# Kernel optimization log

Measured on AMD Instinct MI355X. Metric: run time of the kernel, lower is better.

Reference implementation:

```python
import jax, jax.numpy as jnp
import numpy as np

EMBED = 1024
HEADS = 16
HEAD_DIM = EMBED // HEADS


def setup_inputs() -> dict:
    key = jax.random.key(0)
    ks = jax.random.split(key, 6)
    B, S = 4, 2048
    scale = 1.0 / np.sqrt(EMBED)
    x = jax.random.normal(ks[0], (B, S, EMBED), dtype=jnp.float32)
    Wq = jax.random.normal(ks[1], (EMBED, EMBED), dtype=jnp.float32) * scale
    Wk = jax.random.normal(ks[2], (EMBED, EMBED), dtype=jnp.float32) * scale
    Wv = jax.random.normal(ks[3], (EMBED, EMBED), dtype=jnp.float32) * scale
    Wo = jax.random.normal(ks[4], (EMBED, EMBED), dtype=jnp.float32) * scale
    bo = jnp.zeros((EMBED,), dtype=jnp.float32)
    return {"x": x, "Wq": Wq, "Wk": Wk, "Wv": Wv, "Wo": Wo, "bo": bo}


def reference(x, Wq, Wk, Wv, Wo, bo):
    B, S, E = x.shape
    H, D = HEADS, HEAD_DIM
    # nn.Linear(no bias): y = x @ W.T ; then split heads -> [B,H,S,D]
    q = (x @ Wq.T).reshape(B, S, H, D).transpose(0, 2, 1, 3)
    k = (x @ Wk.T).reshape(B, S, H, D).transpose(0, 2, 1, 3)
    v = (x @ Wv.T).reshape(B, S, H, D).transpose(0, 2, 1, 3)
    # scores [B,H,S,S] with causal mask (tril)
    energy = jnp.einsum('bhqd,bhkd->bhqk', q, k) / jnp.sqrt(jnp.float32(D))
    causal = jnp.tril(jnp.ones((S, S), dtype=bool))
    energy = jnp.where(causal[None, None], energy, jnp.float32(-jnp.inf))
    attn = jax.nn.softmax(energy, axis=-1)
    # dropout is identity in eval / p used here = 0.0
    out = jnp.einsum('bhqk,bhkd->bhqd', attn, v)
    out = out.transpose(0, 2, 1, 3).reshape(B, S, E)
    return out @ Wo.T + bo
```

## Files before the change

kernel.cpp:

```cpp
#include <hip/hip_runtime.h>
#include <math.h>

#define EMBED 1024
#define HEADS 16
#define HDIM  64
#define SEQ   2048
#define BATCH 4
#define QBLK  128
#define KVBLK 128
#define NQT   (SEQ / QBLK)
#define QSCALE 0.18033688011112042f

typedef __attribute__((ext_vector_type(8))) short short8;
typedef __attribute__((ext_vector_type(4))) float f32x4;
typedef __attribute__((ext_vector_type(16))) float f32x16;
typedef __attribute__((ext_vector_type(2))) unsigned int uint2v;

__device__ __forceinline__ unsigned short f2b(float f) {
    union { float f; unsigned int u; } c; c.f = f;
    unsigned int r = (c.u + 0x7fffu + ((c.u >> 16) & 1u)) >> 16;
    return (unsigned short)r;
}

__device__ __forceinline__ unsigned int cvtpk(float lo, float hi) {
    unsigned int r;
    asm("v_cvt_pk_bf16_f32 %0, %1, %2" : "=v"(r) : "v"(lo), "v"(hi));
    return r;
}

__device__ __forceinline__ void gld16(const void* g, void* l) {
    __builtin_amdgcn_global_load_lds((__attribute__((address_space(1))) void*)g,
                                     (__attribute__((address_space(3))) void*)l,
                                     16, 0, 0);
}

__device__ __forceinline__ f32x16 zero16() {
    f32x16 z;
#pragma unroll
    for (int i = 0; i < 16; ++i) z[i] = 0.f;
    return z;
}

__device__ __forceinline__ void makePB(const f32x16 s, short8& f0, short8& f1) {
    union { unsigned int u[4]; short8 s8; } t;
    {
        unsigned int A0 = cvtpk(s[0], s[1]), A1 = cvtpk(s[2], s[3]);
        unsigned int B0 = cvtpk(s[4], s[5]), B1 = cvtpk(s[6], s[7]);
        uint2v w0 = __builtin_amdgcn_permlane32_swap(A0, B0, false, false);
        uint2v w1 = __builtin_amdgcn_permlane32_swap(A1, B1, false, false);
        t.u[0] = w0[0]; t.u[1] = w1[0]; t.u[2] = w0[1]; t.u[3] = w1[1];
        f0 = t.s8;
    }
    {
        unsigned int A0 = cvtpk(s[8], s[9]), A1 = cvtpk(s[10], s[11]);
        unsigned int B0 = cvtpk(s[12], s[13]), B1 = cvtpk(s[14], s[15]);
        uint2v w0 = __builtin_amdgcn_permlane32_swap(A0, B0, false, false);
        uint2v w1 = __builtin_amdgcn_permlane32_swap(A1, B1, false, false);
        t.u[0] = w0[0]; t.u[1] = w1[0]; t.u[2] = w0[1]; t.u[3] = w1[1];
        f1 = t.s8;
    }
}

__global__ __launch_bounds__(256) void cast_all(const float* __restrict__ x,
                                                const float* __restrict__ wq,
                                                const float* __restrict__ wk,
                                                const float* __restrict__ wv,
                                                const float* __restrict__ wo,
                                                unsigned short* __restrict__ xb,
                                                unsigned short* __restrict__ wqkv,
                                                unsigned short* __restrict__ wob) {
    const int WNblk = 512;
    int b = blockIdx.x;
    const float* src;
    unsigned short* dst;
    int off;
    if (b < 4096)            { src = x;  dst = xb;                    off = b; }
    else if (b < 4096 + WNblk)   { src = wq; dst = wqkv;              off = b - 4096; }
    else if (b < 4096 + 2*WNblk) { src = wk; dst = wqkv + 1024*1024;  off = b - 4096 - WNblk; }
    else if (b < 4096 + 3*WNblk) { src = wv; dst = wqkv + 2*1024*1024; off = b - 4096 - 2*WNblk; }
    else                     { src = wo; dst = wob;                   off = b - 4096 - 3*WNblk; }
    int i = (off * 256 + threadIdx.x) * 8;
    float4 a = *(const float4*)(src + i);
    float4 c = *(const float4*)(src + i + 4);
    short8 v;
    v[0] = (short)f2b(a.x); v[1] = (short)f2b(a.y);
    v[2] = (short)f2b(a.z); v[3] = (short)f2b(a.w);
    v[4] = (short)f2b(c.x); v[5] = (short)f2b(c.y);
    v[6] = (short)f2b(c.z); v[7] = (short)f2b(c.w);
    *(short8*)(dst + i) = v;
}

template <int MODE>
__global__ __launch_bounds__(256) void gemm_bf16(const unsigned short* __restrict__ A,
                                                 const unsigned short* __restrict__ W,
                                                 void* __restrict__ outp,
                                                 const float* __restrict__ bias) {
    const int K_ = EMBED;
    __shared__ __attribute__((aligned(16))) unsigned short As[128 * 32];
    __shared__ __attribute__((aligned(16))) unsigned short Bs[128 * 32];

    const int tid  = threadIdx.x;
    const int lane = tid & 63;
    const int w    = tid >> 6;
    const int wr   = w >> 1, wc = w & 1;

    const int nbx = (MODE == 0) ? 24 : 8;
    const int cpx = (MODE == 0) ? 192 : 64;
    const int nb  = (blockIdx.x & 7) * cpx + (blockIdx.x >> 3);
    const int m0 = (nb / nbx) * 128, n0 = (nb % nbx) * 128;

    const unsigned short* gA = A + (size_t)(m0 + w * 32 + (lane >> 2)) * K_ + (lane & 3) * 8;
    const unsigned short* gB = W + (size_t)(n0 + w * 32 + (lane >> 2)) * K_ + (lane & 3) * 8;
    unsigned short* lA = As + (w * 32) * 32;
    unsigned short* lB = Bs + (w * 32) * 32;

    f32x4 zero = {0.f, 0.f, 0.f, 0.f};
    f32x4 acc[4][4];
#pragma unroll
    for (int i = 0; i < 4; ++i)
#pragma unroll
        for (int j = 0; j < 4; ++j) acc[i][j] = zero;

    for (int k0 = 0; k0 < K_; k0 += 32) {
        gld16(gA, lA);
        gld16(gA + (size_t)16 * K_, lA + 16 * 32);
        gld16(gB, lB);
        gld16(gB + (size_t)16 * K_, lB + 16 * 32);
        gA += 32; gB += 32;
        __syncthreads();
        short8 af[4], bfr[4];
#pragma unroll
        for (int i = 0; i < 4; ++i) {
            af[i]  = *(const short8*)&As[(wr * 64 + i * 16 + (lane & 15)) * 32 + (lane >> 4) * 8];
            bfr[i] = *(const short8*)&Bs[(wc * 64 + i * 16 + (lane & 15)) * 32 + (lane >> 4) * 8];
        }
#pragma unroll
        for (int i = 0; i < 4; ++i)
#pragma unroll
            for (int j = 0; j < 4; ++j)
                acc[i][j] = __builtin_amdgcn_mfma_f32_16x16x32_bf16(af[i], bfr[j], acc[i][j], 0, 0, 0);
        __syncthreads();
    }

    if (MODE == 0) {
        const size_t PP = (size_t)BATCH * SEQ * EMBED;
        unsigned short* dst = (unsigned short*)outp;
#pragma unroll
        for (int i = 0; i < 4; ++i)
#pragma unroll
            for (int ni = 0; ni < 4; ++ni) {
                int n = n0 + wc * 64 + ni * 16 + (lane & 15);
                int which = n >> 10;
                int h = (n >> 6) & 15, d = n & 63;
                float os = (which == 0) ? QSCALE : 1.0f;
#pragma unroll
                for (int j = 0; j < 4; ++j) {
                    int m = m0 + wr * 64 + i * 16 + (lane >> 4) * 4 + j;
                    int b = m >> 11, s = m & (SEQ - 1);
                    dst[(size_t)which * PP + (((size_t)b * HEADS + h) * SEQ + s) * HDIM + d] =
                        f2b(acc[i][ni][j] * os);
                }
            }
    } else {
        float* dst = (float*)outp;
#pragma unroll
        for (int i = 0; i < 4; ++i)
#pragma unroll
            for (int ni = 0; ni < 4; ++ni) {
                int n = n0 + wc * 64 + ni * 16 + (lane & 15);
                float bv = bias[n];
#pragma unroll
                for (int j = 0; j < 4; ++j) {
                    int m = m0 + wr * 64 + i * 16 + (lane >> 4) * 4 + j;
                    dst[(size_t)m * EMBED + n] = acc[i][ni][j] + bv;
                }
            }
    }
}

__global__ __launch_bounds__(256, 2) void attn_mfma32(const unsigned short* __restrict__ Q,
                                                      const unsigned short* __restrict__ K,
                                                      const unsigned short* __restrict__ V,
                                                      unsigned short* __restrict__ att) {
    __shared__ __attribute__((aligned(16))) unsigned short KsL[2][KVBLK * 64];
    __shared__ __attribute__((aligned(16))) unsigned short VtL[2][64 * KVBLK];

    const int tid  = threadIdx.x;
    const int lane = tid & 63;
    const int wv   = tid >> 6;
    const int hi   = lane >> 5;
    const int lq   = lane & 31;
    const int bid  = blockIdx.x;
    const int pair = bid >> 6;
    const int bh   = (bid & 7) * 8 + ((bid >> 3) & 7);
    const int qtA  = (NQT - 1) - pair;
    const int qtB  = pair;
    const size_t base = (size_t)bh * SEQ * HDIM;

    const int krow = tid >> 3;
    const int kxor = ((tid & 7) ^ (krow & 7)) * 8;
    const int vkp = tid & 63, vo = (tid >> 6) * 2;
    const int ksw = (lq & 7) << 4;

    short8 ones;
#pragma unroll
    for (int e = 0; e < 8; ++e) ones[e] = (short)0x3F80;

    short8 qf[4];
    auto loadQ = [&](int qt) {
        const unsigned short* qrow =
            Q + base + (size_t)(qt * QBLK + wv * 32 + lq) * HDIM + hi * 8;
        qf[0] = *(const short8*)(qrow);
        qf[1] = *(const short8*)(qrow + 16);
        qf[2] = *(const short8*)(qrow + 32);
        qf[3] = *(const short8*)(qrow + 48);
    };

    auto stageK = [&](int k0, int bufi) {
        const unsigned short* g0 = K + base + (size_t)(k0 + krow) * HDIM + kxor;
        unsigned short* l0 = &KsL[bufi][wv * 512];
#pragma unroll
        for (int j = 0; j < 4; ++j)
            gld16(g0 + (size_t)(32 * j) * HDIM, l0 + j * 2048);
    };

    short8 va0, vb0, va1, vb1;
    auto loadV = [&](int k0) {
        const unsigned short* vp = V + base + (size_t)(k0 + 2 * vkp) * HDIM;
        va0 = *(const short8*)(vp + vo * 8);
        vb0 = *(const short8*)(vp + HDIM + vo * 8);
        va1 = *(const short8*)(vp + (vo + 1) * 8);
        vb1 = *(const short8*)(vp + HDIM + (vo + 1) * 8);
    };
    auto writeV = [&](int bufi) {
        char* vb_ = (char*)&VtL[bufi][0];
#pragma unroll
        for (int e = 0; e < 8; ++e) {
            unsigned int p0 = (unsigned int)(unsigned short)va0[e] |
                              ((unsigned int)(unsigned short)vb0[e] << 16);
            *(unsigned int*)(vb_ + ((vo * 8 + e) << 8) + ((4 * vkp) ^ (e << 4))) = p0;
            unsigned int p1 = (unsigned int)(unsigned short)va1[e] |
                              ((unsigned int)(unsigned short)vb1[e] << 16);
            *(unsigned int*)(vb_ + (((vo + 1) * 8 + e) << 8) + ((4 * vkp) ^ (e << 4))) = p1;
        }
    };

    f32x16 o0 = zero16(), o1 = zero16(), oL = zero16();

    const int b_ = bh >> 4, h_ = bh & 15;
    auto writeOut = [&](int q0w_) {
        const float invl = 1.f / oL[0];
        unsigned short* orow =
            att + ((size_t)b_ * SEQ + (q0w_ + lq)) * EMBED + h_ * HDIM + 4 * hi;
#pragma unroll
        for (int c = 0; c < 4; ++c) {
            unsigned int w0 = cvtpk(o0[4 * c] * invl, o0[4 * c + 1] * invl);
            unsigned int w1 = cvtpk(o0[4 * c + 2] * invl, o0[4 * c + 3] * invl);
            *(uint2*)(orow + 8 * c) = make_uint2(w0, w1);
            unsigned int w2 = cvtpk(o1[4 * c] * invl, o1[4 * c + 1] * invl);
            unsigned int w3 = cvtpk(o1[4 * c + 2] * invl, o1[4 * c + 3] * invl);
            *(uint2*)(orow + 32 + 8 * c) = make_uint2(w2, w3);
        }
    };

    loadQ(qtA);
    int qtCur = qtA;
    int q0w = qtA * QBLK + wv * 32;
    int qsel = q0w + lq;
    stageK(0, 0);
    loadV(0);
    writeV(0);
    __syncthreads();

    const int niter = NQT + 1;
    for (int i = 0; i < niter; ++i) {
        const int buf = i & 1, nbuf = buf ^ 1;
        const int kt = (i <= qtA) ? i : (i - qtA - 1);
        const int k0 = kt * KVBLK;
        const bool pf = (i + 1 < niter);

        if (pf) {
            const int ktN = (i + 1 <= qtA) ? (i + 1) : (i - qtA);
            stageK(ktN * KVBLK, nbuf);
            loadV(ktN * KVBLK);
        }

        const char* kbase = (const char*)&KsL[buf][0];
        f32x16 sS[4];
        __builtin_amdgcn_s_setprio(1);
#pragma unroll
        for (int c = 0; c < 4; ++c) {
            const char* kb_ = kbase + ((c * 32 + lq) << 7);
            f32x16 acc = zero16();
#pragma unroll
            for (int dc = 0; dc < 4; ++dc) {
                short8 kf = *(const short8*)(kb_ + ((((dc << 1) | hi) << 4) ^ ksw));
                acc = __builtin_amdgcn_mfma_f32_32x32x16_bf16(kf, qf[dc], acc, 0, 0, 0);
            }
            sS[c] = acc;
        }
        __builtin_amdgcn_s_setprio(0);

        if (kt == qtCur) {
#pragma unroll
            for (int c = 0; c < 4; ++c)
#pragma unroll
                for (int r = 0; r < 16; ++r) {
                    int key = k0 + 32 * c + (r & 3) + 8 * (r >> 2) + 4 * hi;
                    if (key > qsel) sS[c][r] = -INFINITY;
                }
        }

        const char* vtb = (const char*)&VtL[buf][0];
        __builtin_amdgcn_s_setprio(1);
#pragma unroll
        for (int c = 0; c < 4; ++c) {
#pragma unroll
            for (int r = 0; r < 16; ++r)
                sS[c][r] = __builtin_exp2f(sS[c][r]);
            short8 pb0, pb1;
            makePB(sS[c], pb0, pb1);
            short8 vf;
            vf = *(const short8*)(vtb + (lq << 8) + ((c * 64 + hi * 16) ^ ksw));
            o0 = __builtin_amdgcn_mfma_f32_32x32x16_bf16(vf, pb0, o0, 0, 0, 0);
            vf = *(const short8*)(vtb + (lq << 8) + ((c * 64 + 32 + hi * 16) ^ ksw));
            o0 = __builtin_amdgcn_mfma_f32_32x32x16_bf16(vf, pb1, o0, 0, 0, 0);
            vf = *(const short8*)(vtb + ((32 + lq) << 8) + ((c * 64 + hi * 16) ^ ksw));
            o1 = __builtin_amdgcn_mfma_f32_32x32x16_bf16(vf, pb0, o1, 0, 0, 0);
            vf = *(const short8*)(vtb + ((32 + lq) << 8) + ((c * 64 + 32 + hi * 16) ^ ksw));
            o1 = __builtin_amdgcn_mfma_f32_32x32x16_bf16(vf, pb1, o1, 0, 0, 0);
            oL = __builtin_amdgcn_mfma_f32_32x32x16_bf16(ones, pb0, oL, 0, 0, 0);
            oL = __builtin_amdgcn_mfma_f32_32x32x16_bf16(ones, pb1, oL, 0, 0, 0);
        }
        __builtin_amdgcn_s_setprio(0);

        if (pf) writeV(nbuf);
        __syncthreads();

        if (i == qtA) {
            writeOut(q0w);
            o0 = zero16(); o1 = zero16(); oL = zero16();
            loadQ(qtB);
            qtCur = qtB;
            q0w = qtB * QBLK + wv * 32;
            qsel = q0w + lq;
        }
    }
    writeOut(q0w);
}

extern "C" void kernel_launch(void* const* d_in, const int* in_sizes, int n_in,
                              void* d_out, int out_size, void* d_ws, size_t ws_size,
                              hipStream_t stream) {
    const float* x  = (const float*)d_in[0];
    const float* Wq = (const float*)d_in[1];
    const float* Wk = (const float*)d_in[2];
    const float* Wv = (const float*)d_in[3];
    const float* Wo = (const float*)d_in[4];
    const float* bo = (const float*)d_in[5];

    const size_t XN = (size_t)BATCH * SEQ * EMBED;
    const size_t WN = (size_t)EMBED * EMBED;

    unsigned short* ws   = (unsigned short*)d_ws;
    unsigned short* xb   = ws;
    unsigned short* wqkv = xb + XN;
    unsigned short* wob  = wqkv + 3 * WN;
    unsigned short* Qb   = wob + WN;
    unsigned short* attb = Qb + 3 * XN;

    cast_all<<<4096 + 4 * 512, 256, 0, stream>>>(x, Wq, Wk, Wv, Wo, xb, wqkv, wob);

    gemm_bf16<0><<<1536, 256, 0, stream>>>(xb, wqkv, Qb, nullptr);

    attn_mfma32<<<(NQT / 2) * BATCH * HEADS, 256, 0, stream>>>(
        Qb, Qb + XN, Qb + 2 * XN, attb);

    gemm_bf16<1><<<512, 256, 0, stream>>>(attb, wob, d_out, bo);
}
```

Measured before the change: 171.6 us.

## Store V pre-transposed from projection and skip masked diagonal tiles

The QKV projection epilogue now writes V in a transposed [B,H,D,S] layout. The attention kernel can then stage V into LDS with async global-to-LDS copies like K, instead of doing register loads followed by a scalar transpose-and-write. On diagonal KV tiles, each wave also skips the 32-key chunks that lie wholly above its causal boundary and masks only the partially covered chunk. The cost is a strided, less coalesced V store in the projection epilogue and extra divergent-looking control flow in the attention loop.

```diff
diff --git a/kernel.cpp b/kernel.cpp
--- a/kernel.cpp
+++ b/kernel.cpp
@@ -157,8 +157,14 @@
                 for (int j = 0; j < 4; ++j) {
                     int m = m0 + wr * 64 + i * 16 + (lane >> 4) * 4 + j;
                     int b = m >> 11, s = m & (SEQ - 1);
-                    dst[(size_t)which * PP + (((size_t)b * HEADS + h) * SEQ + s) * HDIM + d] =
-                        f2b(acc[i][ni][j] * os);
+                    if (which == 2) {
+                        dst[2 * PP + (((size_t)b * HEADS + h) * HDIM + d) * SEQ + s] =
+                            f2b(acc[i][ni][j]);
+                    } else {
+                        dst[(size_t)which * PP +
+                            (((size_t)b * HEADS + h) * SEQ + s) * HDIM + d] =
+                            f2b(acc[i][ni][j] * os);
+                    }
                 }
             }
     } else {
@@ -180,7 +186,7 @@
 
 __global__ __launch_bounds__(256, 2) void attn_mfma32(const unsigned short* __restrict__ Q,
                                                       const unsigned short* __restrict__ K,
-                                                      const unsigned short* __restrict__ V,
+                                                      const unsigned short* __restrict__ Vt,
                                                       unsigned short* __restrict__ att) {
     __shared__ __attribute__((aligned(16))) unsigned short KsL[2][KVBLK * 64];
     __shared__ __attribute__((aligned(16))) unsigned short VtL[2][64 * KVBLK];
@@ -199,7 +205,6 @@
 
     const int krow = tid >> 3;
     const int kxor = ((tid & 7) ^ (krow & 7)) * 8;
-    const int vkp = tid & 63, vo = (tid >> 6) * 2;
     const int ksw = (lq & 7) << 4;
 
     short8 ones;
@@ -224,25 +229,14 @@
             gld16(g0 + (size_t)(32 * j) * HDIM, l0 + j * 2048);
     };
 
-    short8 va0, vb0, va1, vb1;
-    auto loadV = [&](int k0) {
-        const unsigned short* vp = V + base + (size_t)(k0 + 2 * vkp) * HDIM;
-        va0 = *(const short8*)(vp + vo * 8);
-        vb0 = *(const short8*)(vp + HDIM + vo * 8);
-        va1 = *(const short8*)(vp + (vo + 1) * 8);
-        vb1 = *(const short8*)(vp + HDIM + (vo + 1) * 8);
-    };
-    auto writeV = [&](int bufi) {
-        char* vb_ = (char*)&VtL[bufi][0];
-#pragma unroll
-        for (int e = 0; e < 8; ++e) {
-            unsigned int p0 = (unsigned int)(unsigned short)va0[e] |
-                              ((unsigned int)(unsigned short)vb0[e] << 16);
-            *(unsigned int*)(vb_ + ((vo * 8 + e) << 8) + ((4 * vkp) ^ (e << 4))) = p0;
-            unsigned int p1 = (unsigned int)(unsigned short)va1[e] |
-                              ((unsigned int)(unsigned short)vb1[e] << 16);
-            *(unsigned int*)(vb_ + (((vo + 1) * 8 + e) << 8) + ((4 * vkp) ^ (e << 4))) = p1;
-        }
+    const int vd0 = wv * 4 + (lane >> 4);
+    auto stageV = [&](int k0, int bufi) {
+        const char* g0 = (const char*)(Vt + base + (size_t)vd0 * SEQ + k0) +
+                         (((lane & 15) * 16) ^ ((vd0 & 7) << 4));
+        unsigned short* l0 = &VtL[bufi][wv * 512];
+#pragma unroll
+        for (int j = 0; j < 4; ++j)
+            gld16(g0 + (size_t)(16 * j) * (SEQ * 2), l0 + j * 2048);
     };
 
     f32x16 o0 = zero16(), o1 = zero16(), oL = zero16();
@@ -268,8 +262,7 @@
     int q0w = qtA * QBLK + wv * 32;
     int qsel = q0w + lq;
     stageK(0, 0);
-    loadV(0);
-    writeV(0);
+    stageV(0, 0);
     __syncthreads();
 
     const int niter = NQT + 1;
@@ -282,59 +275,68 @@
         if (pf) {
             const int ktN = (i + 1 <= qtA) ? (i + 1) : (i - qtA);
             stageK(ktN * KVBLK, nbuf);
-            loadV(ktN * KVBLK);
-        }
+            stageV(ktN * KVBLK, nbuf);
+        }
+
+        const bool diag = (kt == qtCur);
+        const int cmax = diag ? wv : 3;
 
         const char* kbase = (const char*)&KsL[buf][0];
         f32x16 sS[4];
         __builtin_amdgcn_s_setprio(1);
 #pragma unroll
         for (int c = 0; c < 4; ++c) {
-            const char* kb_ = kbase + ((c * 32 + lq) << 7);
-            f32x16 acc = zero16();
-#pragma unroll
-            for (int dc = 0; dc < 4; ++dc) {
-                short8 kf = *(const short8*)(kb_ + ((((dc << 1) | hi) << 4) ^ ksw));
-                acc = __builtin_amdgcn_mfma_f32_32x32x16_bf16(kf, qf[dc], acc, 0, 0, 0);
-            }
-            sS[c] = acc;
+            if (c <= cmax) {
+                const char* kb_ = kbase + ((c * 32 + lq) << 7);
+                f32x16 acc = zero16();
+#pragma unroll
+                for (int dc = 0; dc < 4; ++dc) {
+                    short8 kf = *(const short8*)(kb_ + ((((dc << 1) | hi) << 4) ^ ksw));
+                    acc = __builtin_amdgcn_mfma_f32_32x32x16_bf16(kf, qf[dc], acc, 0, 0, 0);
+                }
+                sS[c] = acc;
+            }
         }
         __builtin_amdgcn_s_setprio(0);
 
-        if (kt == qtCur) {
-#pragma unroll
-            for (int c = 0; c < 4; ++c)
-#pragma unroll
-                for (int r = 0; r < 16; ++r) {
-                    int key = k0 + 32 * c + (r & 3) + 8 * (r >> 2) + 4 * hi;
-                    if (key > qsel) sS[c][r] = -INFINITY;
+        if (diag) {
+#pragma unroll
+            for (int c = 0; c < 4; ++c) {
+                if (c == wv) {
+#pragma unroll
+                    for (int r = 0; r < 16; ++r) {
+                        int key = k0 + 32 * c + (r & 3) + 8 * (r >> 2) + 4 * hi;
+                        if (key > qsel) sS[c][r] = -INFINITY;
+                    }
                 }
+            }
         }
 
         const char* vtb = (const char*)&VtL[buf][0];
         __builtin_amdgcn_s_setprio(1);
 #pragma unroll
         for (int c = 0; c < 4; ++c) {
-#pragma unroll
-            for (int r = 0; r < 16; ++r)
-                sS[c][r] = __builtin_exp2f(sS[c][r]);
-            short8 pb0, pb1;
-            makePB(sS[c], pb0, pb1);
-            short8 vf;
-            vf = *(const short8*)(vtb + (lq << 8) + ((c * 64 + hi * 16) ^ ksw));
-            o0 = __builtin_amdgcn_mfma_f32_32x32x16_bf16(vf, pb0, o0, 0, 0, 0);
-            vf = *(const short8*)(vtb + (lq << 8) + ((c * 64 + 32 + hi * 16) ^ ksw));
-            o0 = __builtin_amdgcn_mfma_f32_32x32x16_bf16(vf, pb1, o0, 0, 0, 0);
-            vf = *(const short8*)(vtb + ((32 + lq) << 8) + ((c * 64 + hi * 16) ^ ksw));
-            o1 = __builtin_amdgcn_mfma_f32_32x32x16_bf16(vf, pb0, o1, 0, 0, 0);
-            vf = *(const short8*)(vtb + ((32 + lq) << 8) + ((c * 64 + 32 + hi * 16) ^ ksw));
-            o1 = __builtin_amdgcn_mfma_f32_32x32x16_bf16(vf, pb1, o1, 0, 0, 0);
-            oL = __builtin_amdgcn_mfma_f32_32x32x16_bf16(ones, pb0, oL, 0, 0, 0);
-            oL = __builtin_amdgcn_mfma_f32_32x32x16_bf16(ones, pb1, oL, 0, 0, 0);
+            if (c <= cmax) {
+#pragma unroll
+                for (int r = 0; r < 16; ++r)
+                    sS[c][r] = __builtin_exp2f(sS[c][r]);
+                short8 pb0, pb1;
+                makePB(sS[c], pb0, pb1);
+                short8 vf;
+                vf = *(const short8*)(vtb + (lq << 8) + ((c * 64 + hi * 16) ^ ksw));
+                o0 = __builtin_amdgcn_mfma_f32_32x32x16_bf16(vf, pb0, o0, 0, 0, 0);
+                vf = *(const short8*)(vtb + (lq << 8) + ((c * 64 + 32 + hi * 16) ^ ksw));
+                o0 = __builtin_amdgcn_mfma_f32_32x32x16_bf16(vf, pb1, o0, 0, 0, 0);
+                vf = *(const short8*)(vtb + ((32 + lq) << 8) + ((c * 64 + hi * 16) ^ ksw));
+                o1 = __builtin_amdgcn_mfma_f32_32x32x16_bf16(vf, pb0, o1, 0, 0, 0);
+                vf = *(const short8*)(vtb + ((32 + lq) << 8) + ((c * 64 + 32 + hi * 16) ^ ksw));
+                o1 = __builtin_amdgcn_mfma_f32_32x32x16_bf16(vf, pb1, o1, 0, 0, 0);
+                oL = __builtin_amdgcn_mfma_f32_32x32x16_bf16(ones, pb0, oL, 0, 0, 0);
+                oL = __builtin_amdgcn_mfma_f32_32x32x16_bf16(ones, pb1, oL, 0, 0, 0);
+            }
         }
         __builtin_amdgcn_s_setprio(0);
 
-        if (pf) writeV(nbuf);
         __syncthreads();
 
         if (i == qtA) {
```

Result: slower. 197.0 us (+14.8%).

## Halve KV tile to 64 and skip per-wave fully masked causal sub-tiles

Applied to the files above, without the earlier changes.

Shrinks the KV tile from 128 to 64 keys, which halves shared-memory use, and raises the launch-bounds occupancy hint from 2 to 4 blocks per CU. Each wave now checks its own 32-row query slice against the KV tile. It skips tiles and 32-key chunks that lie entirely above the causal diagonal, and applies masking only on tiles that cross it. The cost is twice as many loop iterations and barriers, plus wave-divergent control flow inside a block that shares barriers.

```diff
diff --git a/kernel.cpp b/kernel.cpp
--- a/kernel.cpp
+++ b/kernel.cpp
@@ -7,7 +7,7 @@
 #define SEQ   2048
 #define BATCH 4
 #define QBLK  128
-#define KVBLK 128
+#define KVBLK 64
 #define NQT   (SEQ / QBLK)
 #define QSCALE 0.18033688011112042f
 
@@ -178,7 +178,7 @@
     }
 }
 
-__global__ __launch_bounds__(256, 2) void attn_mfma32(const unsigned short* __restrict__ Q,
+__global__ __launch_bounds__(256, 4) void attn_mfma32(const unsigned short* __restrict__ Q,
                                                       const unsigned short* __restrict__ K,
                                                       const unsigned short* __restrict__ V,
                                                       unsigned short* __restrict__ att) {
@@ -199,7 +199,7 @@
 
     const int krow = tid >> 3;
     const int kxor = ((tid & 7) ^ (krow & 7)) * 8;
-    const int vkp = tid & 63, vo = (tid >> 6) * 2;
+    const int vrp = tid & 31, vo = tid >> 5;
     const int ksw = (lq & 7) << 4;
 
     short8 ones;
@@ -219,29 +219,23 @@
     auto stageK = [&](int k0, int bufi) {
         const unsigned short* g0 = K + base + (size_t)(k0 + krow) * HDIM + kxor;
         unsigned short* l0 = &KsL[bufi][wv * 512];
-#pragma unroll
-        for (int j = 0; j < 4; ++j)
-            gld16(g0 + (size_t)(32 * j) * HDIM, l0 + j * 2048);
-    };
-
-    short8 va0, vb0, va1, vb1;
+        gld16(g0, l0);
+        gld16(g0 + (size_t)32 * HDIM, l0 + 2048);
+    };
+
+    short8 va0, vb0;
     auto loadV = [&](int k0) {
-        const unsigned short* vp = V + base + (size_t)(k0 + 2 * vkp) * HDIM;
-        va0 = *(const short8*)(vp + vo * 8);
-        vb0 = *(const short8*)(vp + HDIM + vo * 8);
-        va1 = *(const short8*)(vp + (vo + 1) * 8);
-        vb1 = *(const short8*)(vp + HDIM + (vo + 1) * 8);
+        const unsigned short* vp = V + base + (size_t)(k0 + 2 * vrp) * HDIM + vo * 8;
+        va0 = *(const short8*)vp;
+        vb0 = *(const short8*)(vp + HDIM);
     };
     auto writeV = [&](int bufi) {
         char* vb_ = (char*)&VtL[bufi][0];
 #pragma unroll
         for (int e = 0; e < 8; ++e) {
-            unsigned int p0 = (unsigned int)(unsigned short)va0[e] |
+            unsigned int pk = (unsigned int)(unsigned short)va0[e] |
                               ((unsigned int)(unsigned short)vb0[e] << 16);
-            *(unsigned int*)(vb_ + ((vo * 8 + e) << 8) + ((4 * vkp) ^ (e << 4))) = p0;
-            unsigned int p1 = (unsigned int)(unsigned short)va1[e] |
-                              ((unsigned int)(unsigned short)vb1[e] << 16);
-            *(unsigned int*)(vb_ + (((vo + 1) * 8 + e) << 8) + ((4 * vkp) ^ (e << 4))) = p1;
+            *(unsigned int*)(vb_ + ((vo * 8 + e) << 7) + ((4 * vrp) ^ (e << 4))) = pk;
         }
     };
 
@@ -264,7 +258,6 @@
     };
 
     loadQ(qtA);
-    int qtCur = qtA;
     int q0w = qtA * QBLK + wv * 32;
     int qsel = q0w + lq;
     stageK(0, 0);
@@ -272,76 +265,90 @@
     writeV(0);
     __syncthreads();
 
-    const int niter = NQT + 1;
+    const int nA = 2 * qtA + 2;
+    const int niter = 2 * NQT + 2;
     for (int i = 0; i < niter; ++i) {
         const int buf = i & 1, nbuf = buf ^ 1;
-        const int kt = (i <= qtA) ? i : (i - qtA - 1);
+        const int kt = (i < nA) ? i : (i - nA);
         const int k0 = kt * KVBLK;
         const bool pf = (i + 1 < niter);
 
         if (pf) {
-            const int ktN = (i + 1 <= qtA) ? (i + 1) : (i - qtA);
+            const int ktN = (i + 1 < nA) ? (i + 1) : (i + 1 - nA);
             stageK(ktN * KVBLK, nbuf);
             loadV(ktN * KVBLK);
         }
 
-        const char* kbase = (const char*)&KsL[buf][0];
-        f32x16 sS[4];
-        __builtin_amdgcn_s_setprio(1);
-#pragma unroll
-        for (int c = 0; c < 4; ++c) {
-            const char* kb_ = kbase + ((c * 32 + lq) << 7);
-            f32x16 acc = zero16();
-#pragma unroll
-            for (int dc = 0; dc < 4; ++dc) {
-                short8 kf = *(const short8*)(kb_ + ((((dc << 1) | hi) << 4) ^ ksw));
-                acc = __builtin_amdgcn_mfma_f32_32x32x16_bf16(kf, qf[dc], acc, 0, 0, 0);
-            }
-            sS[c] = acc;
-        }
-        __builtin_amdgcn_s_setprio(0);
-
-        if (kt == qtCur) {
-#pragma unroll
-            for (int c = 0; c < 4; ++c)
-#pragma unroll
-                for (int r = 0; r < 16; ++r) {
-                    int key = k0 + 32 * c + (r & 3) + 8 * (r >> 2) + 4 * hi;
-                    if (key > qsel) sS[c][r] = -INFINITY;
-                }
-        }
-
-        const char* vtb = (const char*)&VtL[buf][0];
-        __builtin_amdgcn_s_setprio(1);
-#pragma unroll
-        for (int c = 0; c < 4; ++c) {
-#pragma unroll
-            for (int r = 0; r < 16; ++r)
-                sS[c][r] = __builtin_exp2f(sS[c][r]);
-            short8 pb0, pb1;
-            makePB(sS[c], pb0, pb1);
-            short8 vf;
-            vf = *(const short8*)(vtb + (lq << 8) + ((c * 64 + hi * 16) ^ ksw));
-            o0 = __builtin_amdgcn_mfma_f32_32x32x16_bf16(vf, pb0, o0, 0, 0, 0);
-            vf = *(const short8*)(vtb + (lq << 8) + ((c * 64 + 32 + hi * 16) ^ ksw));
-            o0 = __builtin_amdgcn_mfma_f32_32x32x16_bf16(vf, pb1, o0, 0, 0, 0);
-            vf = *(const short8*)(vtb + ((32 + lq) << 8) + ((c * 64 + hi * 16) ^ ksw));
-            o1 = __builtin_amdgcn_mfma_f32_32x32x16_bf16(vf, pb0, o1, 0, 0, 0);
-            vf = *(const short8*)(vtb + ((32 + lq) << 8) + ((c * 64 + 32 + hi * 16) ^ ksw));
-            o1 = __builtin_amdgcn_mfma_f32_32x32x16_bf16(vf, pb1, o1, 0, 0, 0);
-            oL = __builtin_amdgcn_mfma_f32_32x32x16_bf16(ones, pb0, oL, 0, 0, 0);
-            oL = __builtin_amdgcn_mfma_f32_32x32x16_bf16(ones, pb1, oL, 0, 0, 0);
-        }
-        __builtin_amdgcn_s_setprio(0);
+        const int rel = (q0w + 31 - k0);
+        const bool active = (rel >= 0);
+        if (active) {
+            const int cmax = (rel >> 5) > 1 ? 1 : (rel >> 5);
+            const bool partial = (k0 + 63 > q0w);
+
+            const char* kbase = (const char*)&KsL[buf][0];
+            f32x16 sS[2];
+            __builtin_amdgcn_s_setprio(1);
+#pragma unroll
+            for (int c = 0; c < 2; ++c) {
+                if (c <= cmax) {
+                    const char* kb_ = kbase + ((c * 32 + lq) << 7);
+                    f32x16 acc = zero16();
+#pragma unroll
+                    for (int dc = 0; dc < 4; ++dc) {
+                        short8 kf = *(const short8*)(kb_ + ((((dc << 1) | hi) << 4) ^ ksw));
+                        acc = __builtin_amdgcn_mfma_f32_32x32x16_bf16(kf, qf[dc], acc, 0, 0, 0);
+                    }
+                    sS[c] = acc;
+                }
+            }
+            __builtin_amdgcn_s_setprio(0);
+
+            if (partial) {
+#pragma unroll
+                for (int c = 0; c < 2; ++c) {
+                    if (c <= cmax) {
+#pragma unroll
+                        for (int r = 0; r < 16; ++r) {
+                            int key = k0 + 32 * c + (r & 3) + 8 * (r >> 2) + 4 * hi;
+                            if (key > qsel) sS[c][r] = -INFINITY;
+                        }
+                    }
+                }
+            }
+
+            const char* vtb = (const char*)&VtL[buf][0];
+            __builtin_amdgcn_s_setprio(1);
+#pragma unroll
+            for (int c = 0; c < 2; ++c) {
+                if (c <= cmax) {
+#pragma unroll
+                    for (int r = 0; r < 16; ++r)
+                        sS[c][r] = __builtin_exp2f(sS[c][r]);
+                    short8 pb0, pb1;
+                    makePB(sS[c], pb0, pb1);
+                    short8 vf;
+                    vf = *(const short8*)(vtb + (lq << 7) + ((c * 64 + hi * 16) ^ ksw));
+                    o0 = __builtin_amdgcn_mfma_f32_32x32x16_bf16(vf, pb0, o0, 0, 0, 0);
+                    vf = *(const short8*)(vtb + (lq << 7) + ((c * 64 + 32 + hi * 16) ^ ksw));
+                    o0 = __builtin_amdgcn_mfma_f32_32x32x16_bf16(vf, pb1, o0, 0, 0, 0);
+                    vf = *(const short8*)(vtb + ((32 + lq) << 7) + ((c * 64 + hi * 16) ^ ksw));
+                    o1 = __builtin_amdgcn_mfma_f32_32x32x16_bf16(vf, pb0, o1, 0, 0, 0);
+                    vf = *(const short8*)(vtb + ((32 + lq) << 7) + ((c * 64 + 32 + hi * 16) ^ ksw));
+                    o1 = __builtin_amdgcn_mfma_f32_32x32x16_bf16(vf, pb1, o1, 0, 0, 0);
+                    oL = __builtin_amdgcn_mfma_f32_32x32x16_bf16(ones, pb0, oL, 0, 0, 0);
+                    oL = __builtin_amdgcn_mfma_f32_32x32x16_bf16(ones, pb1, oL, 0, 0, 0);
+                }
+            }
+            __builtin_amdgcn_s_setprio(0);
+        }
 
         if (pf) writeV(nbuf);
         __syncthreads();
 
-        if (i == qtA) {
+        if (i == nA - 1) {
             writeOut(q0w);
             o0 = zero16(); o1 = zero16(); oL = zero16();
             loadQ(qtB);
-            qtCur = qtB;
             q0w = qtB * QBLK + wv * 32;
             qsel = q0w + lq;
         }
```

Measured after the change: 225.0 us. 31.1% more time.
